# Optimization experiments

Measured on AMD Instinct MI355X. Metric: run time of the kernel, lower is better.

The kernel has to match this reference:

```python
import jax, jax.numpy as jnp
import numpy as np

K = 8                      # neighbors per node (module default)
MUL0, MUL1, MUL2 = 64, 32, 16   # multiplicities of 0e, 1o, 2e
D = MUL0 + 3 * MUL1 + 5 * MUL2  # 240 = irreps dim


def _w3j_112():
    """Wigner-3j-like coupling 1 x 1 -> 2 (real basis), Frobenius norm 1 like e3nn."""
    M = np.zeros((5, 3, 3), dtype=np.float32)
    s = 1.0 / np.sqrt(2.0)
    M[0, 0, 1] = M[0, 1, 0] = s          # xy
    M[1, 0, 2] = M[1, 2, 0] = s          # xz
    M[2, 1, 2] = M[2, 2, 1] = s          # yz
    M[3, 0, 0] = s; M[3, 1, 1] = -s      # x^2 - y^2
    t = 1.0 / np.sqrt(6.0)
    M[4, 0, 0] = -t; M[4, 1, 1] = -t; M[4, 2, 2] = 2 * t  # 2z^2 - x^2 - y^2
    return jnp.asarray(np.transpose(M, (1, 2, 0)) / np.sqrt(5.0))  # [3,3,5]

C112 = _w3j_112()                         # coupling for 1o x 1o -> 2e
C211 = jnp.transpose(C112, (2, 0, 1))     # cyclic permutation: 2e x 1o -> 1o


def _knn_edges(coords, k):
    """Per-batch kNN graph; returns flat (senders, receivers) into [B*N] node ids."""
    B, N, _ = coords.shape
    d2 = jnp.sum((coords[:, :, None, :] - coords[:, None, :, :]) ** 2, -1)  # [B,N,N]
    d2 = d2 + jnp.eye(N, dtype=coords.dtype) * 1e9  # exclude self
    _, nbr = jax.lax.top_k(-d2, k)                  # [B,N,k] neighbor indices
    offs = (jnp.arange(B) * N)[:, None, None]
    senders = (nbr + offs).reshape(-1)
    receivers = jnp.broadcast_to(jnp.arange(N)[None, :, None] + offs, (B, N, k)).reshape(-1)
    return senders, receivers


def setup_inputs() -> dict:
    key = jax.random.key(0)
    ks = jax.random.split(key, 9)
    B, N = 4, 4096
    return {
        "node_feats": jax.random.normal(ks[0], (B, N, D), jnp.float32),
        "coords": jax.random.normal(ks[1], (B, N, 3), jnp.float32) * 10.0,
        "W1": jax.random.normal(ks[2], (MUL0, MUL1), jnp.float32),  # 0e x 1o -> 1o
        "W2": jax.random.normal(ks[3], (MUL1, MUL0), jnp.float32),  # 1o x 1o -> 0e
        "W3": jax.random.normal(ks[4], (MUL1, MUL2), jnp.float32),  # 1o x 1o -> 2e
        "W4": jax.random.normal(ks[5], (MUL2, MUL1), jnp.float32),  # 2e x 1o -> 1o
        "L0": jax.random.normal(ks[6], (MUL0, MUL0), jnp.float32),
        "L1": jax.random.normal(ks[7], (MUL1, MUL1), jnp.float32),
        "L2": jax.random.normal(ks[8], (MUL2, MUL2), jnp.float32),
    }


def reference(node_feats, coords, W1, W2, W3, W4, L0, L1, L2):
    B, N, _ = node_feats.shape
    senders, receivers = _knn_edges(coords, K)
    cf = coords.reshape(-1, 3)
    ev = cf[senders] - cf[receivers]              # [E,3] edge vectors (1x1o)
    xj = node_feats.reshape(-1, D)[senders]       # per-edge gather of sender feats
    x0 = xj[:, :MUL0]                             # [E,64]   0e
    x1 = xj[:, MUL0:MUL0 + 3 * MUL1].reshape(-1, MUL1, 3)  # [E,32,3] 1o
    x2 = xj[:, MUL0 + 3 * MUL1:].reshape(-1, MUL2, 5)      # [E,16,5] 2e

    # FullyConnectedTensorProduct (component irrep norm, 'element' path norm)
    # fan_in to 1o output: MUL0 + MUL2 = 80; to 0e: 32; to 2e: 32.
    m1 = jnp.sqrt(1.0 / (MUL0 + MUL2)) * jnp.einsum('eu,ek,uw->ewk', x0, ev, W1)
    m1 = m1 + jnp.sqrt(3.0 / (MUL0 + MUL2)) * jnp.einsum('eua,ajk,ej,uw->ewk', x2, C211, ev, W4)
    m0 = jnp.sqrt(1.0 / (3.0 * MUL1)) * jnp.einsum('eui,ei,uw->ew', x1, ev, W2)
    m2 = jnp.sqrt(5.0 / MUL1) * jnp.einsum('eui,ej,ijk,uw->ewk', x1, ev, C112, W3)
    msg = jnp.concatenate([m0, m1.reshape(-1, 3 * MUL1), m2.reshape(-1, 5 * MUL2)], axis=-1)

    # scatter-add aggregation at receivers
    agg = jax.ops.segment_sum(msg, receivers, num_segments=B * N)  # [B*N, D]

    # equivariant Linear: per-irrep multiplicity mixing, fan_in-normalized
    y0 = (agg[:, :MUL0] @ L0) / jnp.sqrt(float(MUL0))
    y1 = jnp.einsum('nuk,uw->nwk', agg[:, MUL0:MUL0 + 3 * MUL1].reshape(-1, MUL1, 3), L1) / jnp.sqrt(float(MUL1))
    y2 = jnp.einsum('nuk,uw->nwk', agg[:, MUL0 + 3 * MUL1:].reshape(-1, MUL2, 5), L2) / jnp.sqrt(float(MUL2))
    out = jnp.concatenate([y0, y1.reshape(-1, 3 * MUL1), y2.reshape(-1, 5 * MUL2)], axis=-1)
    return out.reshape(B, N, D)
```

## Files before the change

kernel.cpp:

```cpp
#include <hip/hip_runtime.h>

#define NN   4096
#define KNBR 8
#define DF   240
#define NSUB 16
#define QPB  64

__device__ __forceinline__ void insD9(float v, float t[9]) {
#pragma unroll
  for (int k = 8; k >= 1; k--)
    t[k] = __builtin_amdgcn_fmed3f(t[k - 1], t[k], v);
  t[0] = fminf(t[0], v);
}

__device__ __forceinline__ void insertDI(float d2, int j, float bd[KNBR],
                                         int bi[KNBR]) {
#pragma unroll
  for (int k = KNBR - 1; k >= 1; k--) {
    bool mk  = d2 < bd[k];
    bool mk1 = d2 < bd[k - 1];
    bd[k] = mk ? (mk1 ? bd[k - 1] : d2) : bd[k];
    bi[k] = mk ? (mk1 ? bi[k - 1] : j) : bi[k];
  }
  bool m0 = d2 < bd[0];
  bd[0] = m0 ? d2 : bd[0];
  bi[0] = m0 ? j : bi[0];
}

__global__ __launch_bounds__(1024) void knn_all(
    const float* __restrict__ coords,
    const float* __restrict__ W1, const float* __restrict__ W2,
    const float* __restrict__ W3, const float* __restrict__ W4,
    const float* __restrict__ L0, const float* __restrict__ L1,
    const float* __restrict__ L2, float* __restrict__ Wf,
    int* __restrict__ nbr) {
  if (blockIdx.x >= 256) {
    const float sA = 0.012757759076995719f;
    const float sB = 0.019764235376052370f;
    const float sC = 0.034232659844072875f;
    const float sD = 0.098821176880261850f;
    int idx = (blockIdx.x - 256) * 1024 + threadIdx.x;
    if (idx < 2048) {
      int u = idx >> 6, c = idx & 63;
      float a = 0.f;
#pragma unroll 8
      for (int m = 0; m < 64; m++) a += W2[u * 64 + m] * L0[m * 64 + c];
      Wf[idx] = sA * a;
    } else if (idx < 4096) {
      int t = idx - 2048;
      int u = t >> 5, c = t & 31;
      float a = 0.f;
#pragma unroll 8
      for (int m = 0; m < 32; m++) a += W1[u * 32 + m] * L1[m * 32 + c];
      Wf[idx] = sB * a;
    } else if (idx < 4608) {
      int t = idx - 4096;
      int u = t >> 5, c = t & 31;
      float a = 0.f;
#pragma unroll 8
      for (int m = 0; m < 32; m++) a += W4[u * 32 + m] * L1[m * 32 + c];
      Wf[idx] = sC * a;
    } else {
      int t = idx - 4608;
      int u = t >> 4, c = t & 15;
      float a = 0.f;
#pragma unroll 8
      for (int m = 0; m < 16; m++) a += W3[u * 16 + m] * L2[m * 16 + c];
      Wf[idx] = sD * a;
    }
    return;
  }

  __shared__ float4 cnd[3072];
  __shared__ float pd[NSUB][QPB][9];
  __shared__ unsigned short pi[NSUB][QPB][9];
  __shared__ float thrS[QPB];

  const int blk = blockIdx.x;
  const int b = blk >> 6;
  const int chunk = blk & 63;
  const int qi  = threadIdx.x & 63;
  const int sub = threadIdx.x >> 6;
  const int iq  = chunk * 64 + qi;
  const float* cb = coords + (size_t)b * NN * 3;
  const float4* cb4 = (const float4*)cb;

  {
    int t = threadIdx.x;
    cnd[t]        = cb4[t];
    cnd[1024 + t] = cb4[1024 + t];
    cnd[2048 + t] = cb4[2048 + t];
  }
  const float qx = cb[iq * 3 + 0], qy = cb[iq * 3 + 1], qz = cb[iq * 3 + 2];
  __syncthreads();

  const int j0 = sub * 256;

  float t0v = 3.0e38f, t1v = 3.0e38f;
#pragma unroll 8
  for (int g = 0; g < 64; ++g) {
    int f = 3 * (sub * 64 + g);
    float4 f0 = cnd[f + 0];
    float4 f1 = cnd[f + 1];
    float4 f2 = cnd[f + 2];
    float xs[4] = {f0.x, f0.w, f1.z, f2.y};
    float ys[4] = {f0.y, f1.x, f1.w, f2.z};
    float zs[4] = {f0.z, f1.y, f2.x, f2.w};
#pragma unroll
    for (int c = 0; c < 4; ++c) {
      float dx = xs[c] - qx, dy = ys[c] - qy, dz = zs[c] - qz;
      float d2 = dx * dx + dy * dy + dz * dz;
      t1v = __builtin_amdgcn_fmed3f(t0v, t1v, d2);
      t0v = fminf(t0v, d2);
    }
  }
  pd[sub][qi][0] = t0v;
  pd[sub][qi][1] = t1v;
  __syncthreads();

  if (threadIdx.x < 64) {
    const int q = threadIdx.x;
    float md[9];
#pragma unroll
    for (int k = 0; k < 9; k++) md[k] = 3.0e38f;
    for (int s = 0; s < NSUB; s++) {
      insD9(pd[s][q][0], md);
      insD9(pd[s][q][1], md);
    }
    thrS[q] = md[8];
  }
  __syncthreads();

  const float tq = thrS[qi];
  float bd[KNBR];
  int bi[KNBR];
#pragma unroll
  for (int k = 0; k < KNBR; k++) { bd[k] = 3.0e38f; bi[k] = 0; }
#pragma unroll 2
  for (int g = 0; g < 64; ++g) {
    int base = j0 + 4 * g;
    int f = 3 * (sub * 64 + g);
    float4 f0 = cnd[f + 0];
    float4 f1 = cnd[f + 1];
    float4 f2 = cnd[f + 2];
    float xs[4] = {f0.x, f0.w, f1.z, f2.y};
    float ys[4] = {f0.y, f1.x, f1.w, f2.z};
    float zs[4] = {f0.z, f1.y, f2.x, f2.w};
    float d2s[4];
#pragma unroll
    for (int c = 0; c < 4; ++c) {
      float dx = xs[c] - qx, dy = ys[c] - qy, dz = zs[c] - qz;
      float d2 = dx * dx + dy * dy + dz * dz;
      d2s[c] = (base + c == iq) ? 3.0e38f : d2;
    }
    float m4 = fminf(fminf(d2s[0], d2s[1]), fminf(d2s[2], d2s[3]));
    if (m4 <= tq) {
#pragma unroll
      for (int c = 0; c < 4; ++c)
        if (d2s[c] <= tq) insertDI(d2s[c], base + c, bd, bi);
    }
  }
#pragma unroll
  for (int k = 0; k < KNBR; k++) {
    pd[sub][qi][k] = bd[k];
    pi[sub][qi][k] = (unsigned short)bi[k];
  }
  __syncthreads();

  if (threadIdx.x < 64) {
    const int q = threadIdx.x;
    float md[KNBR];
    int mi[KNBR];
#pragma unroll
    for (int k = 0; k < KNBR; k++) { md[k] = 3.0e38f; mi[k] = 0; }
    for (int s = 0; s < NSUB; s++) {
#pragma unroll
      for (int k = 0; k < KNBR; k++) {
        float vd = pd[s][q][k];
        if (vd < md[KNBR - 1]) insertDI(vd, (int)pi[s][q][k], md, mi);
      }
    }
    int* nr = nbr + (size_t)(b * NN + chunk * 64 + q) * KNBR;
#pragma unroll
    for (int k = 0; k < KNBR; k++) nr[k] = b * NN + mi[k];
  }
}

#define CH_DECL(P)                                                  \
  const float* P##fr[4];                                            \
  float P##xv[4], P##av0[4], P##av1[4], P##av2[4],                  \
        P##bv0[4], P##bv1[4], P##bv2[4], P##bv3[4], P##bv4[4];

#define CH_LOAD(P, H)                                               \
  do {                                                              \
    _Pragma("unroll") for (int i = 0; i < 4; i++) {                 \
      P##fr[i] = feats + (size_t)snbw[4 * (H) + i] * DF;            \
      P##xv[i] = P##fr[i][u];                                       \
    }                                                               \
    if (u < 32) {                                                   \
      _Pragma("unroll") for (int i = 0; i < 4; i++) {               \
        P##av0[i] = P##fr[i][64 + 3 * u];                           \
        P##av1[i] = P##fr[i][65 + 3 * u];                           \
        P##av2[i] = P##fr[i][66 + 3 * u];                           \
      }                                                             \
      if (u < 16) {                                                 \
        _Pragma("unroll") for (int i = 0; i < 4; i++) {             \
          P##bv0[i] = P##fr[i][160 + 5 * u];                        \
          P##bv1[i] = P##fr[i][161 + 5 * u];                        \
          P##bv2[i] = P##fr[i][162 + 5 * u];                        \
          P##bv3[i] = P##fr[i][163 + 5 * u];                        \
          P##bv4[i] = P##fr[i][164 + 5 * u];                        \
        }                                                           \
      }                                                             \
    }                                                               \
  } while (0)

#define CH_CONS(P, H)                                               \
  do {                                                              \
    _Pragma("unroll") for (int i = 0; i < 4; i++) {                 \
      const int e = 4 * (H) + i;                                    \
      float X = sevw[e * 3 + 0];                                    \
      float Y = sevw[e * 3 + 1];                                    \
      float Z = sevw[e * 3 + 2];                                    \
      float sxv = S_ * X, syv = S_ * Y, szv = S_ * Z;               \
      float txv = T_ * X, tyv = T_ * Y, t2z = 2.f * T_ * Z;         \
      z0x += P##xv[i] * X;                                          \
      z0y += P##xv[i] * Y;                                          \
      z0z += P##xv[i] * Z;                                          \
      if (u < 32) {                                                 \
        s1 += P##av0[i] * X + P##av1[i] * Y + P##av2[i] * Z;        \
        p0 += P##av0[i] * syv + P##av1[i] * sxv;                    \
        p1 += P##av0[i] * szv + P##av2[i] * sxv;                    \
        p2 += P##av1[i] * szv + P##av2[i] * syv;                    \
        p3 += P##av0[i] * sxv - P##av1[i] * syv;                    \
        p4 += P##av2[i] * t2z - P##av0[i] * txv - P##av1[i] * tyv;  \
        if (u < 16) {                                               \
          q0 += P##bv0[i] * syv + P##bv1[i] * szv +                 \
                P##bv3[i] * sxv - P##bv4[i] * txv;                  \
          q1 += P##bv0[i] * sxv + P##bv2[i] * szv -                 \
                P##bv3[i] * syv - P##bv4[i] * tyv;                  \
          q2 += P##bv1[i] * sxv + P##bv2[i] * syv + P##bv4[i] * t2z;\
        }                                                           \
      }                                                             \
    }                                                               \
  } while (0)

__global__ __launch_bounds__(256, 4) void msg_kernel(
    const float* __restrict__ feats, const float* __restrict__ coords,
    const int* __restrict__ nbr, const float* __restrict__ Wf,
    float* __restrict__ out) {
  __shared__ float accb[4][432];
  __shared__ float sev[4][KNBR][3];
  __shared__ int snb[4][KNBR];

  const int bid = ((blockIdx.x & 7) << 9) | (blockIdx.x >> 3);
  const int w = threadIdx.x >> 6;
  const int u = threadIdx.x & 63;
  const int node = bid * 4 + w;

  if (u < KNBR) {
    int jg = nbr[(size_t)node * KNBR + u];
    snb[w][u] = jg;
    sev[w][u][0] = coords[(size_t)jg * 3 + 0] - coords[(size_t)node * 3 + 0];
    sev[w][u][1] = coords[(size_t)jg * 3 + 1] - coords[(size_t)node * 3 + 1];
    sev[w][u][2] = coords[(size_t)jg * 3 + 2] - coords[(size_t)node * 3 + 2];
  }
  __syncthreads();

  const float S_ = 0.31622776601683794f;
  const float T_ = 0.18257418583505536f;
  const int* snbw = snb[w];
  const float* sevw = &sev[w][0][0];

  float z0x = 0.f, z0y = 0.f, z0z = 0.f;
  float s1 = 0.f, p0 = 0.f, p1 = 0.f, p2 = 0.f, p3 = 0.f, p4 = 0.f;
  float q0 = 0.f, q1 = 0.f, q2 = 0.f;

  CH_DECL(cA_)
  CH_DECL(cB_)
  CH_LOAD(cA_, 0);
  CH_LOAD(cB_, 1);
  CH_CONS(cA_, 0);
  CH_CONS(cB_, 1);

  float* A = accb[w];
  A[32 + 3 * u + 0] = z0x;
  A[32 + 3 * u + 1] = z0y;
  A[32 + 3 * u + 2] = z0z;
  if (u < 32) {
    A[u] = s1;
    float* pp = A + 224 + 5 * u;
    pp[0] = p0; pp[1] = p1; pp[2] = p2; pp[3] = p3; pp[4] = p4;
  }
  if (u < 16) {
    float* qq = A + 384 + 3 * u;
    qq[0] = q0; qq[1] = q1; qq[2] = q2;
  }
  __syncthreads();

  const float* WA = Wf;
  const float* WB = Wf + 2048;
  const float* WC = Wf + 4096;
  const float* WD = Wf + 4608;
  float* orow = out + (size_t)node * DF;

  {
    float a = 0.f;
#pragma unroll
    for (int m = 0; m < 32; m++) a += A[m] * WA[m * 64 + u];
    orow[u] = a;
  }
#pragma unroll
  for (int m0 = 0; m0 < 96; m0 += 64) {
    int m = m0 + u;
    if (m < 96) {
      int w1 = m / 3, k = m - w1 * 3;
      float a = 0.f;
#pragma unroll
      for (int t = 0; t < 64; t++) a += A[32 + 3 * t + k] * WB[t * 32 + w1];
#pragma unroll
      for (int t = 0; t < 16; t++) a += A[384 + 3 * t + k] * WC[t * 32 + w1];
      orow[64 + m] = a;
    }
  }
#pragma unroll
  for (int m0 = 0; m0 < 80; m0 += 64) {
    int m = m0 + u;
    if (m < 80) {
      int w2 = m / 5, k = m - w2 * 5;
      float a = 0.f;
#pragma unroll
      for (int t = 0; t < 32; t++) a += A[224 + 5 * t + k] * WD[t * 16 + w2];
      orow[160 + m] = a;
    }
  }
}

extern "C" void kernel_launch(void* const* d_in, const int* in_sizes, int n_in,
                              void* d_out, int out_size, void* d_ws,
                              size_t ws_size, hipStream_t stream) {
  const float* feats  = (const float*)d_in[0];
  const float* coords = (const float*)d_in[1];
  const float* W1 = (const float*)d_in[2];
  const float* W2 = (const float*)d_in[3];
  const float* W3 = (const float*)d_in[4];
  const float* W4 = (const float*)d_in[5];
  const float* L0 = (const float*)d_in[6];
  const float* L1 = (const float*)d_in[7];
  const float* L2 = (const float*)d_in[8];
  float* out = (float*)d_out;

  float* Wf  = (float*)d_ws;
  int*   nbr = (int*)((float*)d_ws + 5120);

  knn_all<<<261, 1024, 0, stream>>>(coords, W1, W2, W3, W4, L0, L1, L2, Wf,
                                    nbr);
  msg_kernel<<<4096, 256, 0, stream>>>(feats, coords, nbr, Wf, out);
}
```

Measured before the change: 185.2 us.

## Split kNN candidate set across two blocks and merge partial top-k in message kernel

Each query chunk is now handled by two blocks, each scanning half of the candidate points. With only 256 blocks of 1024 threads before, the GPU was underfilled, and doubling the block count is meant to raise occupancy. Each half writes its partial top-8 distances and indices to workspace. The message kernel then merges the 16 candidates per node with a shuffle-based rank computation. In exchange this adds workspace traffic and merge work in the message kernel, and it changes the threshold logic: a half that does not contain the query uses the 8th-smallest distance rather than the 9th.

```diff
diff --git a/kernel.cpp b/kernel.cpp
--- a/kernel.cpp
+++ b/kernel.cpp
@@ -33,13 +33,13 @@
     const float* __restrict__ W3, const float* __restrict__ W4,
     const float* __restrict__ L0, const float* __restrict__ L1,
     const float* __restrict__ L2, float* __restrict__ Wf,
-    int* __restrict__ nbr) {
-  if (blockIdx.x >= 256) {
+    float* __restrict__ qd2, int* __restrict__ qj2) {
+  if (blockIdx.x >= 512) {
     const float sA = 0.012757759076995719f;
     const float sB = 0.019764235376052370f;
     const float sC = 0.034232659844072875f;
     const float sD = 0.098821176880261850f;
-    int idx = (blockIdx.x - 256) * 1024 + threadIdx.x;
+    int idx = (blockIdx.x - 512) * 1024 + threadIdx.x;
     if (idx < 2048) {
       int u = idx >> 6, c = idx & 63;
       float a = 0.f;
@@ -71,14 +71,15 @@
     return;
   }
 
-  __shared__ float4 cnd[3072];
+  __shared__ float4 cnd[1536];
   __shared__ float pd[NSUB][QPB][9];
   __shared__ unsigned short pi[NSUB][QPB][9];
   __shared__ float thrS[QPB];
 
   const int blk = blockIdx.x;
-  const int b = blk >> 6;
-  const int chunk = blk & 63;
+  const int b = blk >> 7;
+  const int chunk = (blk >> 1) & 63;
+  const int half = blk & 1;
   const int qi  = threadIdx.x & 63;
   const int sub = threadIdx.x >> 6;
   const int iq  = chunk * 64 + qi;
@@ -87,19 +88,17 @@
 
   {
     int t = threadIdx.x;
-    cnd[t]        = cb4[t];
-    cnd[1024 + t] = cb4[1024 + t];
-    cnd[2048 + t] = cb4[2048 + t];
+    const float4* src = cb4 + half * 1536;
+    cnd[t] = src[t];
+    if (t < 512) cnd[1024 + t] = src[1024 + t];
   }
   const float qx = cb[iq * 3 + 0], qy = cb[iq * 3 + 1], qz = cb[iq * 3 + 2];
   __syncthreads();
 
-  const int j0 = sub * 256;
-
   float t0v = 3.0e38f, t1v = 3.0e38f;
 #pragma unroll 8
-  for (int g = 0; g < 64; ++g) {
-    int f = 3 * (sub * 64 + g);
+  for (int g = 0; g < 32; ++g) {
+    int f = 3 * (sub * 32 + g);
     float4 f0 = cnd[f + 0];
     float4 f1 = cnd[f + 1];
     float4 f2 = cnd[f + 2];
@@ -118,7 +117,7 @@
   pd[sub][qi][1] = t1v;
   __syncthreads();
 
-  if (threadIdx.x < 64) {
+  if (threadIdx.x < QPB) {
     const int q = threadIdx.x;
     float md[9];
 #pragma unroll
@@ -127,19 +126,21 @@
       insD9(pd[s][q][0], md);
       insD9(pd[s][q][1], md);
     }
-    thrS[q] = md[8];
+    int iqq = chunk * 64 + q;
+    thrS[q] = ((iqq >> 11) == half) ? md[8] : md[7];
   }
   __syncthreads();
 
   const float tq = thrS[qi];
+  const int jbase = half * 2048 + sub * 128;
   float bd[KNBR];
   int bi[KNBR];
 #pragma unroll
   for (int k = 0; k < KNBR; k++) { bd[k] = 3.0e38f; bi[k] = 0; }
 #pragma unroll 2
-  for (int g = 0; g < 64; ++g) {
-    int base = j0 + 4 * g;
-    int f = 3 * (sub * 64 + g);
+  for (int g = 0; g < 32; ++g) {
+    int base = jbase + 4 * g;
+    int f = 3 * (sub * 32 + g);
     float4 f0 = cnd[f + 0];
     float4 f1 = cnd[f + 1];
     float4 f2 = cnd[f + 2];
@@ -167,7 +168,7 @@
   }
   __syncthreads();
 
-  if (threadIdx.x < 64) {
+  if (threadIdx.x < QPB) {
     const int q = threadIdx.x;
     float md[KNBR];
     int mi[KNBR];
@@ -180,9 +181,12 @@
         if (vd < md[KNBR - 1]) insertDI(vd, (int)pi[s][q][k], md, mi);
       }
     }
-    int* nr = nbr + (size_t)(b * NN + chunk * 64 + q) * KNBR;
-#pragma unroll
-    for (int k = 0; k < KNBR; k++) nr[k] = b * NN + mi[k];
+    size_t g2 = ((size_t)(b * NN + chunk * 64 + q) * 2 + half) * KNBR;
+#pragma unroll
+    for (int k = 0; k < KNBR; k++) {
+      qd2[g2 + k] = md[k];
+      qj2[g2 + k] = mi[k];
+    }
   }
 }
 
@@ -247,8 +251,8 @@
 
 __global__ __launch_bounds__(256, 4) void msg_kernel(
     const float* __restrict__ feats, const float* __restrict__ coords,
-    const int* __restrict__ nbr, const float* __restrict__ Wf,
-    float* __restrict__ out) {
+    const float* __restrict__ qd2, const int* __restrict__ qj2,
+    const float* __restrict__ Wf, float* __restrict__ out) {
   __shared__ float accb[4][432];
   __shared__ float sev[4][KNBR][3];
   __shared__ int snb[4][KNBR];
@@ -257,13 +261,29 @@
   const int w = threadIdx.x >> 6;
   const int u = threadIdx.x & 63;
   const int node = bid * 4 + w;
-
-  if (u < KNBR) {
-    int jg = nbr[(size_t)node * KNBR + u];
-    snb[w][u] = jg;
-    sev[w][u][0] = coords[(size_t)jg * 3 + 0] - coords[(size_t)node * 3 + 0];
-    sev[w][u][1] = coords[(size_t)jg * 3 + 1] - coords[(size_t)node * 3 + 1];
-    sev[w][u][2] = coords[(size_t)jg * 3 + 2] - coords[(size_t)node * 3 + 2];
+  const int b = node >> 12;
+
+  float dmy = 3.0e38f;
+  int jmy = 0x7FFFFFFF;
+  if (u < 16) {
+    dmy = qd2[(size_t)node * 16 + u];
+    jmy = qj2[(size_t)node * 16 + u];
+  }
+  int rank = 0;
+#pragma unroll
+  for (int m = 0; m < 16; m++) {
+    float dm = __shfl(dmy, m);
+    int jm = __shfl(jmy, m);
+    bool less = (dm < dmy) ||
+                (dm == dmy && (jm < jmy || (jm == jmy && m < u)));
+    rank += less ? 1 : 0;
+  }
+  if (u < 16 && rank < KNBR) {
+    int jg = b * NN + jmy;
+    snb[w][rank] = jg;
+    sev[w][rank][0] = coords[(size_t)jg * 3 + 0] - coords[(size_t)node * 3 + 0];
+    sev[w][rank][1] = coords[(size_t)jg * 3 + 1] - coords[(size_t)node * 3 + 1];
+    sev[w][rank][2] = coords[(size_t)jg * 3 + 2] - coords[(size_t)node * 3 + 2];
   }
   __syncthreads();
 
@@ -351,9 +371,10 @@
   float* out = (float*)d_out;
 
   float* Wf  = (float*)d_ws;
-  int*   nbr = (int*)((float*)d_ws + 5120);
-
-  knn_all<<<261, 1024, 0, stream>>>(coords, W1, W2, W3, W4, L0, L1, L2, Wf,
-                                    nbr);
-  msg_kernel<<<4096, 256, 0, stream>>>(feats, coords, nbr, Wf, out);
-}
+  float* qd2 = (float*)d_ws + 5120;
+  int*   qj2 = (int*)((float*)d_ws + 5120 + 262144);
+
+  knn_all<<<517, 1024, 0, stream>>>(coords, W1, W2, W3, W4, L0, L1, L2, Wf,
+                                    qd2, qj2);
+  msg_kernel<<<4096, 256, 0, stream>>>(feats, coords, qd2, qj2, Wf, out);
+}
```

Measured after the change: 210.8 us. 13.9% more time.

## Stage transposed fused weights in LDS and vectorize linear-mix dot products

Applied to the files above, without the earlier changes.

The fused weight matrices are now written transposed by the prep kernel and copied by each msg_kernel block into padded shared memory. The per-node accumulators are laid out component-major with padding, so the output mixing loops can read both operands as float4 from LDS instead of strided scalar global loads. This cuts global and L1 traffic in the epilogue. In exchange, every block pays for about 13.5 KB of weight loads and more shared memory, which may reduce occupancy under the 4-blocks-per-CU launch bound.

```diff
diff --git a/kernel.cpp b/kernel.cpp
--- a/kernel.cpp
+++ b/kernel.cpp
@@ -52,21 +52,21 @@
       float a = 0.f;
 #pragma unroll 8
       for (int m = 0; m < 32; m++) a += W1[u * 32 + m] * L1[m * 32 + c];
-      Wf[idx] = sB * a;
+      Wf[2048 + c * 64 + u] = sB * a;
     } else if (idx < 4608) {
       int t = idx - 4096;
       int u = t >> 5, c = t & 31;
       float a = 0.f;
 #pragma unroll 8
       for (int m = 0; m < 32; m++) a += W4[u * 32 + m] * L1[m * 32 + c];
-      Wf[idx] = sC * a;
+      Wf[4096 + c * 16 + u] = sC * a;
     } else {
       int t = idx - 4608;
       int u = t >> 4, c = t & 15;
       float a = 0.f;
 #pragma unroll 8
       for (int m = 0; m < 16; m++) a += W3[u * 16 + m] * L2[m * 16 + c];
-      Wf[idx] = sD * a;
+      Wf[4608 + c * 32 + u] = sD * a;
     }
     return;
   }
@@ -249,7 +249,8 @@
     const float* __restrict__ feats, const float* __restrict__ coords,
     const int* __restrict__ nbr, const float* __restrict__ Wf,
     float* __restrict__ out) {
-  __shared__ float accb[4][432];
+  __shared__ float accb[4][480];
+  __shared__ float wgt[3392];
   __shared__ float sev[4][KNBR][3];
   __shared__ int snb[4][KNBR];
 
@@ -257,6 +258,27 @@
   const int w = threadIdx.x >> 6;
   const int u = threadIdx.x & 63;
   const int node = bid * 4 + w;
+
+  {
+#pragma unroll
+    for (int i = 0; i < 8; i++) {
+      int idx = threadIdx.x + 256 * i;
+      int w1 = idx >> 6, t = idx & 63;
+      wgt[w1 * 68 + t] = Wf[2048 + idx];
+    }
+#pragma unroll
+    for (int i = 0; i < 2; i++) {
+      int idx = threadIdx.x + 256 * i;
+      int w1 = idx >> 4, t = idx & 15;
+      wgt[2176 + w1 * 20 + t] = Wf[4096 + idx];
+    }
+#pragma unroll
+    for (int i = 0; i < 2; i++) {
+      int idx = threadIdx.x + 256 * i;
+      int w2 = idx >> 5, t = idx & 31;
+      wgt[2816 + w2 * 36 + t] = Wf[4608 + idx];
+    }
+  }
 
   if (u < KNBR) {
     int jg = nbr[(size_t)node * KNBR + u];
@@ -284,24 +306,25 @@
   CH_CONS(cB_, 1);
 
   float* A = accb[w];
-  A[32 + 3 * u + 0] = z0x;
-  A[32 + 3 * u + 1] = z0y;
-  A[32 + 3 * u + 2] = z0z;
+  A[32 + 0 * 68 + u] = z0x;
+  A[32 + 1 * 68 + u] = z0y;
+  A[32 + 2 * 68 + u] = z0z;
   if (u < 32) {
     A[u] = s1;
-    float* pp = A + 224 + 5 * u;
-    pp[0] = p0; pp[1] = p1; pp[2] = p2; pp[3] = p3; pp[4] = p4;
+    A[236 + 0 * 36 + u] = p0;
+    A[236 + 1 * 36 + u] = p1;
+    A[236 + 2 * 36 + u] = p2;
+    A[236 + 3 * 36 + u] = p3;
+    A[236 + 4 * 36 + u] = p4;
   }
   if (u < 16) {
-    float* qq = A + 384 + 3 * u;
-    qq[0] = q0; qq[1] = q1; qq[2] = q2;
+    A[416 + 0 * 20 + u] = q0;
+    A[416 + 1 * 20 + u] = q1;
+    A[416 + 2 * 20 + u] = q2;
   }
   __syncthreads();
 
   const float* WA = Wf;
-  const float* WB = Wf + 2048;
-  const float* WC = Wf + 4096;
-  const float* WD = Wf + 4608;
   float* orow = out + (size_t)node * DF;
 
   {
@@ -316,10 +339,22 @@
     if (m < 96) {
       int w1 = m / 3, k = m - w1 * 3;
       float a = 0.f;
-#pragma unroll
-      for (int t = 0; t < 64; t++) a += A[32 + 3 * t + k] * WB[t * 32 + w1];
-#pragma unroll
-      for (int t = 0; t < 16; t++) a += A[384 + 3 * t + k] * WC[t * 32 + w1];
+      const float4* az = (const float4*)(A + 32 + k * 68);
+      const float4* wz = (const float4*)(wgt + w1 * 68);
+#pragma unroll
+      for (int t4 = 0; t4 < 16; t4++) {
+        float4 v = az[t4], wv = wz[t4];
+        a += v.x * wv.x; a += v.y * wv.y;
+        a += v.z * wv.z; a += v.w * wv.w;
+      }
+      const float4* aq = (const float4*)(A + 416 + k * 20);
+      const float4* wc = (const float4*)(wgt + 2176 + w1 * 20);
+#pragma unroll
+      for (int t4 = 0; t4 < 4; t4++) {
+        float4 v = aq[t4], wv = wc[t4];
+        a += v.x * wv.x; a += v.y * wv.y;
+        a += v.z * wv.z; a += v.w * wv.w;
+      }
       orow[64 + m] = a;
     }
   }
@@ -329,8 +364,14 @@
     if (m < 80) {
       int w2 = m / 5, k = m - w2 * 5;
       float a = 0.f;
-#pragma unroll
-      for (int t = 0; t < 32; t++) a += A[224 + 5 * t + k] * WD[t * 16 + w2];
+      const float4* ap = (const float4*)(A + 236 + k * 36);
+      const float4* wd = (const float4*)(wgt + 2816 + w2 * 36);
+#pragma unroll
+      for (int t4 = 0; t4 < 8; t4++) {
+        float4 v = ap[t4], wv = wd[t4];
+        a += v.x * wv.x; a += v.y * wv.y;
+        a += v.z * wv.z; a += v.w * wv.w;
+      }
       orow[160 + m] = a;
     }
   }
```

After: 170.8 us. -7.7%, faster.
